# Optimization experiments

Measured on AMD Instinct MI355X. Metric: run time of the kernel, lower is better.

Reference implementation:

```python
import jax, jax.numpy as jnp
import numpy as np

B, G, D, H, KD = 32, 512, 128, 4, 32  # batch, graph, embed_dim, n_heads, key_dim=embed//heads
NORM = 1.0 / np.sqrt(KD).astype(np.float32)  # MultiHeadCompat norm_factor = 1/sqrt(key_dim)


def _uniform(k, shape, fan):
    s = 1.0 / np.sqrt(fan).astype(np.float32)
    return jax.random.uniform(k, shape, jnp.float32, -s, s)


def setup_inputs() -> dict:
    key = jax.random.key(0)
    ks = jax.random.split(key, 16)
    inp = {
        "h": jax.random.normal(ks[0], (B, G, D), jnp.float32),
        "pos_pickup": jax.random.randint(ks[1], (B,), 0, G),
        "pos_delivery": jax.random.randint(ks[2], (B,), 0, G),
        "rec": jax.random.randint(ks[3], (B, G), 0, G),
        # compater_insert1 / compater_insert2 projections: (n_heads, input_dim, key_dim)
        "Wq1": _uniform(ks[4], (H, D, KD), KD),
        "Wk1": _uniform(ks[5], (H, D, KD), KD),
        "Wq2": _uniform(ks[6], (H, D, KD), KD),
        "Wk2": _uniform(ks[7], (H, D, KD), KD),
        # agg MLP(16, 32, 32, 1); stored as (in, out) so y = x @ W + b
        "fc1_w": _uniform(ks[8], (16, 32), 16),
        "fc1_b": _uniform(ks[9], (32,), 32),
        "fc2_w": _uniform(ks[10], (32, 32), 32),
        "fc2_b": _uniform(ks[11], (32,), 32),
        "fc3_w": _uniform(ks[12], (32, 1), 32),
        "fc3_b": _uniform(ks[13], (1,), 1),
    }
    return inp


def _compat(qv, hh, Wq, Wk):
    # qv: (B, D) single query node; hh: (B, G, D)
    Q = jnp.einsum('bd,hdk->bhk', qv, Wq)       # (B, H, K)
    K = jnp.einsum('bgd,hdk->bhgk', hh, Wk)     # (B, H, G, K)
    return NORM * jnp.einsum('bhk,bhgk->bgh', Q, K)  # (B, G, H)


def reference(h, pos_pickup, pos_delivery, rec, Wq1, Wk1, Wq2, Wk2,
              fc1_w, fc1_b, fc2_w, fc2_b, fc3_w, fc3_b):
    b, g, d = h.shape
    ar = jnp.arange(b)
    h_pickup = h[ar, pos_pickup]      # (B, D)
    h_delivery = h[ar, pos_delivery]  # (B, D)
    h_neighbour = jnp.take_along_axis(h, rec[:, :, None], axis=1)  # (B, G, D)

    shp = (b, g, g, 4)
    c_pp = jnp.broadcast_to(_compat(h_pickup, h, Wq1, Wk1)[:, :, None, :], shp)
    c_po = jnp.broadcast_to(_compat(h_pickup, h_neighbour, Wq2, Wk2)[:, :, None, :], shp)
    c_dp = jnp.broadcast_to(_compat(h_delivery, h, Wq1, Wk1)[:, None, :, :], shp)
    c_do = jnp.broadcast_to(_compat(h_delivery, h_neighbour, Wq2, Wk2)[:, None, :, :], shp)
    x = jnp.concatenate([c_pp, c_po, c_dp, c_do], axis=-1)  # (B, G, G, 16)

    # agg MLP (dropout p=0.05 is identity at inference)
    x = jax.nn.relu(x @ fc1_w + fc1_b)
    x = jax.nn.relu(x @ fc2_w + fc2_b)
    return (x @ fc3_w + fc3_b)[..., 0]  # (B, G, G)
```

## Files before the change

kernel.cpp:

```cpp
#include <hip/hip_runtime.h>


#define B 32
#define G 512
#define D 128
#define NH 4
#define KD 32
#define NORMF 0.17677669529663687f

#define WS_P16H 131072
#define WS_Q16H 655360

typedef float v16f __attribute__((ext_vector_type(16)));
typedef float f2v __attribute__((ext_vector_type(2)));
typedef _Float16 v8h __attribute__((ext_vector_type(8)));
typedef _Float16 h2v __attribute__((ext_vector_type(2)));

struct HQ { h2v h[4]; };
struct F2x8 { f2v v[8]; };

__device__ __forceinline__ v8h relu_add(const HQ& p, const HQ& q) {
  const h2v z = {(_Float16)0.0f, (_Float16)0.0f};
  HQ r;
#pragma unroll
  for (int i = 0; i < 4; ++i)
    r.h[i] = __builtin_elementwise_max(p.h[i] + q.h[i], z);
  return __builtin_bit_cast(v8h, r);
}

__global__ __launch_bounds__(256) void stage01(
    const float* __restrict__ h, const int* __restrict__ pp,
    const int* __restrict__ pd, const int* __restrict__ rec,
    const float* __restrict__ Wq1, const float* __restrict__ Wk1,
    const float* __restrict__ Wq2, const float* __restrict__ Wk2,
    const float* __restrict__ fc1_w, const float* __restrict__ fc1_b,
    float* __restrict__ ws) {
  const int bx = blockIdx.x;
  const int b = bx >> 3, g0 = (bx & 7) * 64;
  const int t = threadIdx.x;

  __shared__ float hp[D], hd[D];
  __shared__ float qq[4][NH * KD];
  __shared__ float sA[4][NH][D];
  __shared__ float sc[64][17];
  __shared__ float sout[64][33];

  if (t < 128) {
    hp[t] = h[((size_t)b * G + pp[b]) * D + t];
  } else {
    const int u = t - 128;
    hd[u] = h[((size_t)b * G + pd[b]) * D + u];
  }
  __syncthreads();

  if (t < 128) {
    const int hh = t >> 5, k = t & 31;
    const float* wq1 = Wq1 + hh * D * KD + k;
    const float* wq2 = Wq2 + hh * D * KD + k;
    float s1p = 0.f, s2p = 0.f, s1d = 0.f, s2d = 0.f;
    for (int d = 0; d < D; ++d) {
      const float w1 = wq1[d * KD], w2 = wq2[d * KD];
      const float xp = hp[d], xd = hd[d];
      s1p = fmaf(xp, w1, s1p);
      s2p = fmaf(xp, w2, s2p);
      s1d = fmaf(xd, w1, s1d);
      s2d = fmaf(xd, w2, s2d);
    }
    qq[0][t] = s1p; qq[1][t] = s2p; qq[2][t] = s1d; qq[3][t] = s2d;
  }
  __syncthreads();

  {
    const int d = t & 127;
    const int h0 = (t >> 7) * 2;
#pragma unroll
    for (int hh = h0; hh < h0 + 2; ++hh) {
      const float* wk1 = Wk1 + hh * D * KD + d * KD;
      const float* wk2 = Wk2 + hh * D * KD + d * KD;
      float apq = 0.f, apo = 0.f, adp = 0.f, ado = 0.f;
#pragma unroll
      for (int k = 0; k < KD; ++k) {
        const float w1 = wk1[k], w2 = wk2[k];
        apq = fmaf(qq[0][hh * 32 + k], w1, apq);
        adp = fmaf(qq[2][hh * 32 + k], w1, adp);
        apo = fmaf(qq[1][hh * 32 + k], w2, apo);
        ado = fmaf(qq[3][hh * 32 + k], w2, ado);
      }
      sA[0][hh][d] = NORMF * apq;
      sA[1][hh][d] = NORMF * apo;
      sA[2][hh][d] = NORMF * adp;
      sA[3][hh][d] = NORMF * ado;
    }
  }
  __syncthreads();

  const int gl = t & 63;
  const int hh = __builtin_amdgcn_readfirstlane(t >> 6);
  const int g = g0 + gl;
  const float4* hg4 = (const float4*)(h + ((size_t)b * G + g) * D);
  const float4* hn4 = (const float4*)(h + ((size_t)b * G + rec[b * G + g]) * D);

  float cpp = 0.f, cpo = 0.f, cdp = 0.f, cdo = 0.f;
#pragma unroll 4
  for (int d4 = 0; d4 < 32; ++d4) {
    const float4 x = hg4[d4], y = hn4[d4];
    const float4 a1 = *(const float4*)&sA[0][hh][4 * d4];
    const float4 a2 = *(const float4*)&sA[1][hh][4 * d4];
    const float4 a3 = *(const float4*)&sA[2][hh][4 * d4];
    const float4 a4 = *(const float4*)&sA[3][hh][4 * d4];
    cpp = fmaf(x.x, a1.x, fmaf(x.y, a1.y, fmaf(x.z, a1.z, fmaf(x.w, a1.w, cpp))));
    cpo = fmaf(y.x, a2.x, fmaf(y.y, a2.y, fmaf(y.z, a2.z, fmaf(y.w, a2.w, cpo))));
    cdp = fmaf(x.x, a3.x, fmaf(x.y, a3.y, fmaf(x.z, a3.z, fmaf(x.w, a3.w, cdp))));
    cdo = fmaf(y.x, a4.x, fmaf(y.y, a4.y, fmaf(y.z, a4.z, fmaf(y.w, a4.w, cdo))));
  }
  sc[gl][hh] = cpp; sc[gl][4 + hh] = cpo; sc[gl][8 + hh] = cdp; sc[gl][12 + hh] = cdo;
  __syncthreads();

  float u[16];
#pragma unroll
  for (int i = 0; i < 16; ++i) u[i] = sc[gl][i];

  float pv[8], qv[8];
#pragma unroll
  for (int jj = 0; jj < 8; ++jj) {
    const int j = hh * 8 + jj;
    float p = 0.f, q = fc1_b[j];
#pragma unroll
    for (int i = 0; i < 8; ++i) {
      p = fmaf(u[i], fc1_w[i * 32 + j], p);
      q = fmaf(u[8 + i], fc1_w[(8 + i) * 32 + j], q);
    }
    pv[jj] = p; qv[jj] = q;
  }

#pragma unroll
  for (int jj = 0; jj < 8; ++jj) sout[gl][hh * 8 + jj] = pv[jj];
  __syncthreads();
  {
    unsigned* dst = (unsigned*)((unsigned short*)ws + WS_P16H) +
                    ((size_t)b * G + g0) * 16;
#pragma unroll
    for (int i = t; i < 1024; i += 256) {
      const int row = i >> 4, c0 = (2 * i) & 31;
      __fp16 __attribute__((ext_vector_type(2))) pk =
          __builtin_amdgcn_cvt_pkrtz(sout[row][c0], sout[row][c0 + 1]);
      dst[i] = *(const unsigned*)&pk;
    }
  }
  __syncthreads();
#pragma unroll
  for (int jj = 0; jj < 8; ++jj) sout[gl][hh * 8 + jj] = qv[jj];
  __syncthreads();
  {
    unsigned* dst = (unsigned*)((unsigned short*)ws + WS_Q16H) +
                    ((size_t)b * G + g0) * 16;
#pragma unroll
    for (int i = t; i < 1024; i += 256) {
      const int row = i >> 4, c0 = (2 * i) & 31;
      __fp16 __attribute__((ext_vector_type(2))) pk =
          __builtin_amdgcn_cvt_pkrtz(sout[row][c0], sout[row][c0 + 1]);
      dst[i] = *(const unsigned*)&pk;
    }
  }
}

__global__ __launch_bounds__(256, 2) void mlp_pairs(
    const float* __restrict__ ws,
    const float* __restrict__ fc2_w, const float* __restrict__ fc2_b,
    const float* __restrict__ fc3_w, const float* __restrict__ fc3_b,
    float* __restrict__ out) {
  const int b = blockIdx.z;
  const int g1_0 = blockIdx.y * 16;
  const int g2_0 = blockIdx.x * 256;
  const int t = threadIdx.x;
  const int w = t >> 6, l = t & 63;
  const int col = l & 31;
  const int half = l >> 5;
  const int kb = half * 8;

  __shared__ __align__(16) unsigned short sPh[16 * 32];
  {
    const unsigned* Psrc = (const unsigned*)((const unsigned short*)ws + WS_P16H) +
                           ((size_t)b * G + g1_0) * 16;
    ((unsigned*)sPh)[t] = Psrc[t];
  }

  v8h A0, A1;
#pragma unroll
  for (int j = 0; j < 8; ++j) {
    A0[j] = (_Float16)fc2_w[(kb + j) * 32 + col];
    A1[j] = (_Float16)fc2_w[(16 + kb + j) * 32 + col];
  }
  v16f biasC;
  F2x8 w3p;
#pragma unroll
  for (int r = 0; r < 16; ++r) {
    const int n = (r & 3) + 8 * (r >> 2) + 4 * half;
    biasC[r] = fc2_b[n];
    ((float*)&w3p)[r] = fc3_w[n];
  }
  const float b3 = fc3_b[0];

  HQ qlo[2], qhi[2];
#pragma unroll
  for (int c = 0; c < 2; ++c) {
    const unsigned short* qp = (const unsigned short*)ws + WS_Q16H +
        ((size_t)b * G + g2_0 + (2 * w + c) * 32 + col) * 32;
    qlo[c] = __builtin_bit_cast(HQ, *(const uint4*)(qp + kb));
    qhi[c] = __builtin_bit_cast(HQ, *(const uint4*)(qp + 16 + kb));
  }
  __syncthreads();

  const f2v z2 = {0.f, 0.f};
  float* op = out + (((size_t)b * G + g1_0) * G) + g2_0 + w * 64 + half * 32 + col;
#pragma unroll
  for (int i = 0; i < 8; ++i) {
    const int ra = 2 * i, rb = 2 * i + 1;
    const HQ palo = __builtin_bit_cast(HQ, *(const uint4*)(sPh + ra * 32 + kb));
    const HQ pahi = __builtin_bit_cast(HQ, *(const uint4*)(sPh + ra * 32 + 16 + kb));
    const HQ pblo = __builtin_bit_cast(HQ, *(const uint4*)(sPh + rb * 32 + kb));
    const HQ pbhi = __builtin_bit_cast(HQ, *(const uint4*)(sPh + rb * 32 + 16 + kb));

    const v8h Ba0lo = relu_add(palo, qlo[0]);
    const v8h Ba0hi = relu_add(pahi, qhi[0]);
    const v8h Ba1lo = relu_add(palo, qlo[1]);
    const v8h Ba1hi = relu_add(pahi, qhi[1]);
    const v8h Bb0lo = relu_add(pblo, qlo[0]);
    const v8h Bb0hi = relu_add(pbhi, qhi[0]);
    const v8h Bb1lo = relu_add(pblo, qlo[1]);
    const v8h Bb1hi = relu_add(pbhi, qhi[1]);

    v16f aa0 = __builtin_amdgcn_mfma_f32_32x32x16_f16(A0, Ba0lo, biasC, 0, 0, 0);
    v16f aa1 = __builtin_amdgcn_mfma_f32_32x32x16_f16(A0, Ba1lo, biasC, 0, 0, 0);
    v16f ab0 = __builtin_amdgcn_mfma_f32_32x32x16_f16(A0, Bb0lo, biasC, 0, 0, 0);
    v16f ab1 = __builtin_amdgcn_mfma_f32_32x32x16_f16(A0, Bb1lo, biasC, 0, 0, 0);
    aa0 = __builtin_amdgcn_mfma_f32_32x32x16_f16(A1, Ba0hi, aa0, 0, 0, 0);
    aa1 = __builtin_amdgcn_mfma_f32_32x32x16_f16(A1, Ba1hi, aa1, 0, 0, 0);
    ab0 = __builtin_amdgcn_mfma_f32_32x32x16_f16(A1, Bb0hi, ab0, 0, 0, 0);
    ab1 = __builtin_amdgcn_mfma_f32_32x32x16_f16(A1, Bb1hi, ab1, 0, 0, 0);

    const F2x8 fa0 = __builtin_bit_cast(F2x8, aa0);
    const F2x8 fa1 = __builtin_bit_cast(F2x8, aa1);
    const F2x8 fb0 = __builtin_bit_cast(F2x8, ab0);
    const F2x8 fb1 = __builtin_bit_cast(F2x8, ab1);
    f2v ea0 = z2, ea1 = z2, eb0 = z2, eb1 = z2;
#pragma unroll
    for (int k = 0; k < 8; ++k) {
      ea0 = __builtin_elementwise_max(fa0.v[k], z2) * w3p.v[k] + ea0;
      ea1 = __builtin_elementwise_max(fa1.v[k], z2) * w3p.v[k] + ea1;
      eb0 = __builtin_elementwise_max(fb0.v[k], z2) * w3p.v[k] + eb0;
      eb1 = __builtin_elementwise_max(fb1.v[k], z2) * w3p.v[k] + eb1;
    }
    const float sa0 = ea0[0] + ea0[1], sa1 = ea1[0] + ea1[1];
    const float sb0 = eb0[0] + eb0[1], sb1 = eb1[0] + eb1[1];

    float ya = half ? sa1 : sa0;
    float za = half ? sa0 : sa1;
    ya += __shfl_xor(za, 32);
    float yb = half ? sb1 : sb0;
    float zb = half ? sb0 : sb1;
    yb += __shfl_xor(zb, 32);

    op[(size_t)ra * G] = ya + b3;
    op[(size_t)rb * G] = yb + b3;
  }
}

extern "C" void kernel_launch(void* const* d_in, const int* in_sizes, int n_in,
                              void* d_out, int out_size, void* d_ws, size_t ws_size,
                              hipStream_t stream) {
  const float* h     = (const float*)d_in[0];
  const int*   pp    = (const int*)d_in[1];
  const int*   pd    = (const int*)d_in[2];
  const int*   rec   = (const int*)d_in[3];
  const float* Wq1   = (const float*)d_in[4];
  const float* Wk1   = (const float*)d_in[5];
  const float* Wq2   = (const float*)d_in[6];
  const float* Wk2   = (const float*)d_in[7];
  const float* fc1_w = (const float*)d_in[8];
  const float* fc1_b = (const float*)d_in[9];
  const float* fc2_w = (const float*)d_in[10];
  const float* fc2_b = (const float*)d_in[11];
  const float* fc3_w = (const float*)d_in[12];
  const float* fc3_b = (const float*)d_in[13];
  float* out = (float*)d_out;
  float* ws  = (float*)d_ws;

  stage01<<<dim3(256), dim3(256), 0, stream>>>(
      h, pp, pd, rec, Wq1, Wk1, Wq2, Wk2, fc1_w, fc1_b, ws);
  mlp_pairs<<<dim3(2, 32, 32), dim3(256), 0, stream>>>(
      ws, fc2_w, fc2_b, fc3_w, fc3_b, out);
}
```

Baseline: 144.3 us.

## Precompute fp16 fc2 weights in stage01 and double rows per MLP block

Stage01's first block now writes a transposed fp16 copy of fc2_w, plus the permuted fc2 bias and fc3 weights, into the workspace. mlp_pairs then loads them with a few vector loads instead of many scalar loads and conversions per thread. Each mlp_pairs block also handles 32 g1 rows instead of 16, halving the grid so the per-block setup is spread over more work. The tradeoff is fewer blocks in flight, less parallelism, and a small serial write confined to one block of stage01.

```diff
diff --git a/kernel.cpp b/kernel.cpp
--- a/kernel.cpp
+++ b/kernel.cpp
@@ -8,8 +8,10 @@
 #define KD 32
 #define NORMF 0.17677669529663687f
 
-#define WS_P16H 131072
-#define WS_Q16H 655360
+#define WS_BIASF 1024
+#define WS_W3F   1056
+#define WS_P16H  131072
+#define WS_Q16H  655360
 
 typedef float v16f __attribute__((ext_vector_type(16)));
 typedef float f2v __attribute__((ext_vector_type(2)));
@@ -34,10 +36,22 @@
     const float* __restrict__ Wq1, const float* __restrict__ Wk1,
     const float* __restrict__ Wq2, const float* __restrict__ Wk2,
     const float* __restrict__ fc1_w, const float* __restrict__ fc1_b,
+    const float* __restrict__ fc2_w, const float* __restrict__ fc2_b,
+    const float* __restrict__ fc3_w,
     float* __restrict__ ws) {
   const int bx = blockIdx.x;
   const int b = bx >> 3, g0 = (bx & 7) * 64;
   const int t = threadIdx.x;
+
+  if (bx == 0 && t < 32) {
+    _Float16* wt = (_Float16*)ws;
+#pragma unroll
+    for (int k = 0; k < 32; ++k) wt[t * 32 + k] = (_Float16)fc2_w[k * 32 + t];
+    const int r = t & 15, hf = t >> 4;
+    const int n = (r & 3) + 8 * (r >> 2) + 4 * hf;
+    ws[WS_BIASF + t] = fc2_b[n];
+    ws[WS_W3F + t]   = fc3_w[n];
+  }
 
   __shared__ float hp[D], hd[D];
   __shared__ float qq[4][NH * KD];
@@ -165,12 +179,10 @@
 }
 
 __global__ __launch_bounds__(256, 2) void mlp_pairs(
-    const float* __restrict__ ws,
-    const float* __restrict__ fc2_w, const float* __restrict__ fc2_b,
-    const float* __restrict__ fc3_w, const float* __restrict__ fc3_b,
+    const float* __restrict__ ws, const float* __restrict__ fc3_b,
     float* __restrict__ out) {
   const int b = blockIdx.z;
-  const int g1_0 = blockIdx.y * 16;
+  const int g1_0 = blockIdx.y * 32;
   const int g2_0 = blockIdx.x * 256;
   const int t = threadIdx.x;
   const int w = t >> 6, l = t & 63;
@@ -178,27 +190,19 @@
   const int half = l >> 5;
   const int kb = half * 8;
 
-  __shared__ __align__(16) unsigned short sPh[16 * 32];
+  __shared__ __align__(16) unsigned short sPh[32 * 32];
   {
     const unsigned* Psrc = (const unsigned*)((const unsigned short*)ws + WS_P16H) +
                            ((size_t)b * G + g1_0) * 16;
     ((unsigned*)sPh)[t] = Psrc[t];
-  }
-
-  v8h A0, A1;
-#pragma unroll
-  for (int j = 0; j < 8; ++j) {
-    A0[j] = (_Float16)fc2_w[(kb + j) * 32 + col];
-    A1[j] = (_Float16)fc2_w[(16 + kb + j) * 32 + col];
-  }
-  v16f biasC;
-  F2x8 w3p;
-#pragma unroll
-  for (int r = 0; r < 16; ++r) {
-    const int n = (r & 3) + 8 * (r >> 2) + 4 * half;
-    biasC[r] = fc2_b[n];
-    ((float*)&w3p)[r] = fc3_w[n];
-  }
+    ((unsigned*)sPh)[t + 256] = Psrc[t + 256];
+  }
+
+  const unsigned short* wt = (const unsigned short*)ws;
+  const v8h A0 = __builtin_bit_cast(v8h, *(const uint4*)(wt + col * 32 + kb));
+  const v8h A1 = __builtin_bit_cast(v8h, *(const uint4*)(wt + col * 32 + 16 + kb));
+  const v16f biasC = *(const v16f*)(ws + WS_BIASF + half * 16);
+  const F2x8 w3p = __builtin_bit_cast(F2x8, *(const v16f*)(ws + WS_W3F + half * 16));
   const float b3 = fc3_b[0];
 
   HQ qlo[2], qhi[2];
@@ -214,7 +218,7 @@
   const f2v z2 = {0.f, 0.f};
   float* op = out + (((size_t)b * G + g1_0) * G) + g2_0 + w * 64 + half * 32 + col;
 #pragma unroll
-  for (int i = 0; i < 8; ++i) {
+  for (int i = 0; i < 16; ++i) {
     const int ra = 2 * i, rb = 2 * i + 1;
     const HQ palo = __builtin_bit_cast(HQ, *(const uint4*)(sPh + ra * 32 + kb));
     const HQ pahi = __builtin_bit_cast(HQ, *(const uint4*)(sPh + ra * 32 + 16 + kb));
@@ -287,7 +291,6 @@
   float* ws  = (float*)d_ws;
 
   stage01<<<dim3(256), dim3(256), 0, stream>>>(
-      h, pp, pd, rec, Wq1, Wk1, Wq2, Wk2, fc1_w, fc1_b, ws);
-  mlp_pairs<<<dim3(2, 32, 32), dim3(256), 0, stream>>>(
-      ws, fc2_w, fc2_b, fc3_w, fc3_b, out);
-}
+      h, pp, pd, rec, Wq1, Wk1, Wq2, Wk2, fc1_w, fc1_b, fc2_w, fc2_b, fc3_w, ws);
+  mlp_pairs<<<dim3(2, 16, 32), dim3(256), 0, stream>>>(ws, fc3_b, out);
+}
```

After: 143.3 us. About the same (-0.7%).
